# Kernel optimization log

Hardware: AMD Instinct MI355X
Metric: run time of the kernel (lower is better)

## Reference

```python
import jax, jax.numpy as jnp
import numpy as np
from jax.scipy.special import logsumexp

EPS = 0.005
MAX_ITER = 100
TOL = 1e-3
B, N, M, D = 16, 2048, 2048, 3


def setup_inputs() -> dict:
    key = jax.random.key(0)
    k1, k2 = jax.random.split(key)
    p1 = jax.random.normal(k1, (B, N, D), dtype=jnp.float32)
    p2 = jax.random.normal(k2, (B, M, D), dtype=jnp.float32)
    return {"p1": p1, "p2": p2}


def _cdist_l2(p1, p2):
    sq1 = jnp.sum(p1 * p1, axis=-1)                      # (B, N)
    sq2 = jnp.sum(p2 * p2, axis=-1)                      # (B, M)
    cross = jnp.einsum('bnd,bmd->bnm', p1, p2)           # (B, N, M)
    d2 = jnp.maximum(sq1[:, :, None] + sq2[None is None and sq2.ndim and slice(None) or 0][:, None, :] - 2.0 * cross, 0.0) if False else jnp.maximum(sq1[:, :, None] + sq2[:, None, :] - 2.0 * cross, 0.0)
    return jnp.sqrt(d2)


def reference(p1, p2):
    b_, n_, _ = p1.shape
    m_ = p2.shape[1]
    dist = _cdist_l2(p1, p2)                              # (B, N, M)
    log_a = jnp.full((b_, n_), jnp.log(1.0 / n_ + 1e-8), dtype=p1.dtype)
    log_b = jnp.full((b_, m_), jnp.log(1.0 / m_ + 1e-8), dtype=p1.dtype)
    u0 = jnp.zeros((b_, n_), dtype=p1.dtype)
    v0 = jnp.zeros((b_, m_), dtype=p1.dtype)

    def step(carry, _):
        u, v, done = carry
        u_new = EPS * (log_a - logsumexp((v[:, None, :] - dist) / EPS, axis=2))
        v_new = EPS * (log_b - logsumexp((u_new[:, :, None] - dist) / EPS, axis=1))
        conv = (jnp.max(jnp.abs(u_new - u)) < TOL) & (jnp.max(jnp.abs(v_new - v)) < TOL)
        # freeze potentials once converged (emulates the torch early break)
        u = jnp.where(done, u, u_new)
        v = jnp.where(done, v, v_new)
        return (u, v, done | conv), None

    (u, v, _), _ = jax.lax.scan(step, (u0, v0, jnp.array(False)), None, length=MAX_ITER)

    P = jnp.exp((u[:, :, None] + v[:, None, :] - dist) / EPS)  # transport plan
    emd = jnp.sum(P * dist, axis=(1, 2))                       # (B,)
    return jnp.mean(emd)
```

## Files before the change

### kernel.cpp

```cpp
#include <hip/hip_runtime.h>
#include <math.h>

namespace {
constexpr int   Bb    = 16;
constexpr int   Nn    = 2048;
constexpr int   Mm    = 2048;
constexpr float EPSf  = 0.005f;
constexpr int   MAXIT = 100;
constexpr float LN2f  = 0.69314718055994531f;
constexpr float L2Ef  = 1.44269504088896340f;
constexpr float C2f   = 288.53900817779268f;
constexpr int   BLOCK = 256;
constexpr int   RW    = 4;
constexpr int   RPB   = 16;
constexpr int   SUBS  = Nn / RPB;
constexpr int   GRID  = Bb * SUBS;
constexpr int   NCH   = 32;
}

__device__ __forceinline__ float ex2(float x) { return __builtin_amdgcn_exp2f(x); }

__global__ __launch_bounds__(BLOCK) void pack_pts(const float* __restrict__ p,
                                                  float4* __restrict__ pk, int npts) {
  int i = blockIdx.x * BLOCK + threadIdx.x;
  if (i < npts) pk[i] = make_float4(p[3 * i], p[3 * i + 1], p[3 * i + 2], 0.0f);
}

__global__ __launch_bounds__(BLOCK) void bbox_k(const float4* __restrict__ pk1,
                                                const float4* __restrict__ pk2,
                                                float4* __restrict__ bbox) {
  __shared__ float4 smin[BLOCK], smax[BLOCK];
  const int cb = blockIdx.x;
  const float4* p = (cb < 16 ? pk1 : pk2) + (cb & 15) * Nn;
  float4 mn = make_float4(3e38f, 3e38f, 3e38f, 0), mx = make_float4(-3e38f, -3e38f, -3e38f, 0);
  for (int i = threadIdx.x; i < Nn; i += BLOCK) {
    float4 v = p[i];
    mn.x = fminf(mn.x, v.x); mn.y = fminf(mn.y, v.y); mn.z = fminf(mn.z, v.z);
    mx.x = fmaxf(mx.x, v.x); mx.y = fmaxf(mx.y, v.y); mx.z = fmaxf(mx.z, v.z);
  }
  smin[threadIdx.x] = mn; smax[threadIdx.x] = mx;
  __syncthreads();
  for (int k = BLOCK / 2; k > 0; k >>= 1) {
    if (threadIdx.x < k) {
      float4 a = smin[threadIdx.x], c = smin[threadIdx.x + k];
      smin[threadIdx.x] = make_float4(fminf(a.x, c.x), fminf(a.y, c.y), fminf(a.z, c.z), 0);
      float4 d = smax[threadIdx.x], e = smax[threadIdx.x + k];
      smax[threadIdx.x] = make_float4(fmaxf(d.x, e.x), fmaxf(d.y, e.y), fmaxf(d.z, e.z), 0);
    }
    __syncthreads();
  }
  if (threadIdx.x == 0) { bbox[cb * 2] = smin[0]; bbox[cb * 2 + 1] = smax[0]; }
}

__device__ __forceinline__ unsigned spread3(unsigned v) {
  v = (v * 0x00010001u) & 0xFF0000FFu;
  v = (v * 0x00000101u) & 0x0F00F00Fu;
  v = (v * 0x00000011u) & 0xC30C30C3u;
  v = (v * 0x00000005u) & 0x49249249u;
  return v;
}

__global__ __launch_bounds__(BLOCK) void sort_k(float4* __restrict__ pk1,
                                                float4* __restrict__ pk2,
                                                const float4* __restrict__ bbox,
                                                float4* __restrict__ chunkbox) {
  __shared__ float4 pts[Nn];
  __shared__ unsigned key[Nn];
  const int cb = blockIdx.x, tid = threadIdx.x;
  float4* p = (cb < 16 ? pk1 : pk2) + (cb & 15) * Nn;
  float4 lo = bbox[cb * 2], hi = bbox[cb * 2 + 1];
  float sx = 127.0f / fmaxf(hi.x - lo.x, 1e-9f);
  float sy = 127.0f / fmaxf(hi.y - lo.y, 1e-9f);
  float sz = 127.0f / fmaxf(hi.z - lo.z, 1e-9f);
  for (int i = tid; i < Nn; i += BLOCK) {
    float4 v = p[i];
    pts[i] = v;
    unsigned qx = (unsigned)fminf(fmaxf((v.x - lo.x) * sx, 0.f), 127.f);
    unsigned qy = (unsigned)fminf(fmaxf((v.y - lo.y) * sy, 0.f), 127.f);
    unsigned qz = (unsigned)fminf(fmaxf((v.z - lo.z) * sz, 0.f), 127.f);
    unsigned m = spread3(qx) | (spread3(qy) << 1) | (spread3(qz) << 2);
    key[i] = (m << 11) | (unsigned)i;
  }
  __syncthreads();
  for (int k = 2; k <= Nn; k <<= 1)
    for (int j = k >> 1; j > 0; j >>= 1) {
      for (int t = tid; t < Nn / 2; t += BLOCK) {
        int i = ((t & ~(j - 1)) << 1) | (t & (j - 1));
        int ixj = i | j;
        bool up = ((i & k) == 0);
        unsigned a = key[i], bq = key[ixj];
        if ((a > bq) == up) { key[i] = bq; key[ixj] = a; }
      }
      __syncthreads();
    }
  float4 g[Nn / BLOCK];
  #pragma unroll
  for (int c = 0; c < Nn / BLOCK; ++c)
    g[c] = pts[key[tid + c * BLOCK] & 2047u];
  __syncthreads();
  #pragma unroll
  for (int c = 0; c < Nn / BLOCK; ++c) {
    pts[tid + c * BLOCK] = g[c];
    p[tid + c * BLOCK]   = g[c];
  }
  __syncthreads();
  const int lane = tid & 63, wid = tid >> 6;
  for (int c = wid; c < NCH; c += 4) {
    float4 v = pts[c * 64 + lane];
    float mnx = v.x, mny = v.y, mnz = v.z, mxx = v.x, mxy = v.y, mxz = v.z;
    #pragma unroll
    for (int off = 1; off < 64; off <<= 1) {
      mnx = fminf(mnx, __shfl_xor(mnx, off)); mny = fminf(mny, __shfl_xor(mny, off));
      mnz = fminf(mnz, __shfl_xor(mnz, off)); mxx = fmaxf(mxx, __shfl_xor(mxx, off));
      mxy = fmaxf(mxy, __shfl_xor(mxy, off)); mxz = fmaxf(mxz, __shfl_xor(mxz, off));
    }
    if (lane == 0) {
      chunkbox[(cb * NCH + c) * 2]     = make_float4(mnx, mny, mnz, 0);
      chunkbox[(cb * NCH + c) * 2 + 1] = make_float4(mxx, mxy, mxz, 0);
    }
  }
}

__global__ __launch_bounds__(BLOCK, 8) void sink_fast(
    const float4* __restrict__ pkc, float4* __restrict__ pkr,
    float* __restrict__ potr,
    const float4* __restrict__ cbox_cols, const float* __restrict__ cm_cols,
    float* __restrict__ cmout, float thrAdd) {
  __shared__ float redw[4];
  const int tid = threadIdx.x, lane = tid & 63, wid = tid >> 6;
  const int b = blockIdx.x >> 7, sub = blockIdx.x & 127;
  const float4* PC = pkc + b * Mm;
  float4*       PRq = pkr + b * Nn;
  float*        QR  = potr + b * Nn;

  const float log_ab = logf(1.0f / 2048.0f + 1e-8f);
  const float log2ab = log_ab * L2Ef;
  const float invC2 = 1.0f / C2f;

  const int base_n = sub * RPB + wid * RW;
  float qx[RW], qy[RW], qz[RW], K[RW], s[RW];
  #pragma unroll
  for (int r = 0; r < RW; ++r) {
    float4 q = PRq[base_n + r];
    qx[r] = q.x; qy[r] = q.y; qz[r] = q.z;
    K[r]  = log2ab - q.w;
    s[r]  = 0.0f;
  }

  unsigned msk = ~0u;
  if (thrAdd < 1e8f) {
    float4 clo = make_float4(0, 0, 0, 0), chi = clo;
    float cmw = -3.0e38f;
    if (lane < 32) {
      clo = cbox_cols[(b * NCH + lane) * 2];
      chi = cbox_cols[(b * NCH + lane) * 2 + 1];
      float4 c4 = ((const float4*)cm_cols)[b * NCH + lane];
      cmw = fmaxf(fmaxf(c4.x, c4.y), fmaxf(c4.z, c4.w));
    }
    unsigned m = 0;
    #pragma unroll
    for (int r = 0; r < RW; ++r) {
      float thr = (cmw - K[r] + thrAdd) * invC2;
      float ax = fmaxf(fmaxf(clo.x - qx[r], qx[r] - chi.x), 0.0f);
      float ay = fmaxf(fmaxf(clo.y - qy[r], qy[r] - chi.y), 0.0f);
      float az = fmaxf(fmaxf(clo.z - qz[r], qz[r] - chi.z), 0.0f);
      float d2low = fmaf(az, az, fmaf(ay, ay, ax * ax));
      bool keep = (lane < 32) && (thr > 0.0f) && (d2low <= thr * thr);
      m |= (unsigned)(__ballot(keep) & 0xFFFFFFFFull);
    }
    msk = m;
  }

  const float4* p = PC + lane;
  if (msk) {
    int j = __builtin_ctz(msk); msk &= msk - 1;
    float4 f = p[j * 64];
    for (;;) {
      float4 fn; bool more = (msk != 0);
      if (more) { int jn = __builtin_ctz(msk); msk &= msk - 1; fn = p[jn * 64]; }
      #pragma unroll
      for (int r = 0; r < RW; ++r) {
        float dx = f.x - qx[r], dy = f.y - qy[r], dz = f.z - qz[r];
        float d2 = fmaf(dz, dz, fmaf(dy, dy, dx * dx));
        s[r] += ex2(fmaf(__builtin_amdgcn_sqrtf(d2), -C2f, f.w - K[r]));
      }
      if (!more) break;
      f = fn;
    }
  }

  float* PRw = (float*)(PRq);
  float wmax = -3.0e38f;
  #pragma unroll
  for (int r = 0; r < RW; ++r) {
    float sv = s[r];
    #pragma unroll
    for (int off = 1; off < 64; off <<= 1) sv += __shfl_xor(sv, off);
    sv = fmaxf(sv, 1e-37f);
    float lse = (K[r] + __builtin_amdgcn_logf(sv)) * LN2f;
    float pnew = EPSf * (log_ab - lse);
    if (lane == 0) {
      int n = base_n + r;
      __builtin_nontemporal_store(pnew, &QR[n]);
      __builtin_nontemporal_store(pnew * C2f, &PRw[4 * n + 3]);
      wmax = fmaxf(wmax, pnew * C2f);
    }
  }
  if (lane == 0) redw[wid] = wmax;
  __syncthreads();
  if (tid == 0) {
    float m = fmaxf(fmaxf(redw[0], redw[1]), fmaxf(redw[2], redw[3]));
    __builtin_nontemporal_store(m, &cmout[(b * NCH + (sub >> 2)) * 4 + (sub & 3)]);
  }
}

__global__ __launch_bounds__(BLOCK, 8) void final_emd(
    const float4* __restrict__ pk1, const float4* __restrict__ pk2,
    const float* __restrict__ U, float* __restrict__ part) {
  __shared__ float red[4];
  const int tid = threadIdx.x, lane = tid & 63, wid = tid >> 6;
  const int b = blockIdx.x >> 7, sub = blockIdx.x & 127;
  const float4* PC = pk2 + b * Mm;
  const float4* PRq = pk1 + b * Nn;

  const int base_n = sub * RPB + wid * RW;
  float qx[RW], qy[RW], qz[RW], uc[RW], ac[RW];
  #pragma unroll
  for (int r = 0; r < RW; ++r) {
    float4 q = PRq[base_n + r];
    qx[r] = q.x; qy[r] = q.y; qz[r] = q.z;
    uc[r] = U[b * Nn + base_n + r] * C2f;
    ac[r] = 0.0f;
  }

  const float4* p = PC + lane;
  #pragma unroll 2
  for (int j = 0; j < 32; j += 4) {
    float4 f0 = p[(j + 0) * 64];
    float4 f1 = p[(j + 1) * 64];
    float4 f2 = p[(j + 2) * 64];
    float4 f3 = p[(j + 3) * 64];
    #pragma unroll
    for (int r = 0; r < RW; ++r) {
      float dx0 = f0.x - qx[r], dy0 = f0.y - qy[r], dz0 = f0.z - qz[r];
      float dx1 = f1.x - qx[r], dy1 = f1.y - qy[r], dz1 = f1.z - qz[r];
      float dx2 = f2.x - qx[r], dy2 = f2.y - qy[r], dz2 = f2.z - qz[r];
      float dx3 = f3.x - qx[r], dy3 = f3.y - qy[r], dz3 = f3.z - qz[r];
      float e0 = fmaf(dz0, dz0, fmaf(dy0, dy0, dx0 * dx0));
      float e1 = fmaf(dz1, dz1, fmaf(dy1, dy1, dx1 * dx1));
      float e2 = fmaf(dz2, dz2, fmaf(dy2, dy2, dx2 * dx2));
      float e3 = fmaf(dz3, dz3, fmaf(dy3, dy3, dx3 * dx3));
      float t0 = __builtin_amdgcn_sqrtf(e0);
      float t1 = __builtin_amdgcn_sqrtf(e1);
      float t2 = __builtin_amdgcn_sqrtf(e2);
      float t3 = __builtin_amdgcn_sqrtf(e3);
      ac[r] = fmaf(ex2(fmaf(t0, -C2f, f0.w) + uc[r]), t0, ac[r]);
      ac[r] = fmaf(ex2(fmaf(t1, -C2f, f1.w) + uc[r]), t1, ac[r]);
      ac[r] = fmaf(ex2(fmaf(t2, -C2f, f2.w) + uc[r]), t2, ac[r]);
      ac[r] = fmaf(ex2(fmaf(t3, -C2f, f3.w) + uc[r]), t3, ac[r]);
    }
  }
  float acc = 0.0f;
  #pragma unroll
  for (int r = 0; r < RW; ++r) acc += ac[r];
  #pragma unroll
  for (int off = 1; off < 64; off <<= 1) acc += __shfl_xor(acc, off);
  if (lane == 0) red[wid] = acc;
  __syncthreads();
  if (tid == 0) part[blockIdx.x] = (red[0] + red[1]) + (red[2] + red[3]);
}

__global__ __launch_bounds__(BLOCK) void write_out(const float* __restrict__ part,
                                                   float* __restrict__ out) {
  __shared__ double sd[BLOCK];
  int t = threadIdx.x;
  double s = 0.0;
  for (int i = t; i < GRID; i += BLOCK) s += (double)part[i];
  sd[t] = s;
  __syncthreads();
  for (int k = BLOCK / 2; k > 0; k >>= 1) {
    if (t < k) sd[t] += sd[t + k];
    __syncthreads();
  }
  if (t == 0) out[0] = (float)(sd[0] / (double)Bb);
}

extern "C" void kernel_launch(void* const* d_in, const int* in_sizes, int n_in,
                              void* d_out, int out_size, void* d_ws, size_t ws_size,
                              hipStream_t stream) {
  (void)in_sizes; (void)n_in; (void)out_size; (void)ws_size;
  const float* p1 = (const float*)d_in[0];
  const float* p2 = (const float*)d_in[1];
  char* ws = (char*)d_ws;
  float4*   pk1   = (float4*)(ws + 0);
  float4*   pk2   = (float4*)(ws + 524288);
  float*    U     = (float*)(ws + 1048576);
  float*    V     = (float*)(ws + 1179648);
  float*    part  = (float*)(ws + 1310720);
  float4*   bbox  = (float4*)(ws + 1318912);
  float4*   cbox  = (float4*)(ws + 1319936);
  float*    cm    = (float*)(ws + 1352704);
  float4*   cbox1 = cbox;
  float4*   cbox2 = cbox + 16 * NCH * 2;
  float*    cm1   = cm;
  float*    cm2   = cm + 16 * NCH * 4;

  const int npts = Bb * Nn;
  pack_pts<<<(npts + BLOCK - 1) / BLOCK, BLOCK, 0, stream>>>(p1, pk1, npts);
  pack_pts<<<(npts + BLOCK - 1) / BLOCK, BLOCK, 0, stream>>>(p2, pk2, npts);
  bbox_k<<<32, BLOCK, 0, stream>>>(pk1, pk2, bbox);
  sort_k<<<32, BLOCK, 0, stream>>>(pk1, pk2, bbox, cbox);

  sink_fast<<<GRID, BLOCK, 0, stream>>>(pk2, pk1, U, cbox2, cm2, cm1, 1e9f);
  sink_fast<<<GRID, BLOCK, 0, stream>>>(pk1, pk2, V, cbox1, cm1, cm2, 1e9f);
  for (int it = 1; it < MAXIT; ++it) {
    float thr = (it < 4) ? 120.0f : 48.0f;
    sink_fast<<<GRID, BLOCK, 0, stream>>>(pk2, pk1, U, cbox2, cm2, cm1, thr);
    sink_fast<<<GRID, BLOCK, 0, stream>>>(pk1, pk2, V, cbox1, cm1, cm2, thr);
  }

  final_emd<<<GRID, BLOCK, 0, stream>>>(pk1, pk2, U, part);
  write_out<<<1, BLOCK, 0, stream>>>(part, (float*)d_out);
}
```

Before: 4.582 ms.

## Double rows per wave, fuse bbox into sort, fold final reduction into EMD kernel

Raises the number of rows each wave processes from 4 to 8, which halves the grid and doubles column reuse per load. The per-block column-max bookkeeping shrinks from 4 to 2 entries per chunk to match. The separate bbox kernel is merged into the sort kernel using wave shuffles. The write_out kernel is replaced by a last-block ticket reduction inside final_emd, which removes two launches. The trade-off is higher register pressure and fewer blocks (1024) for the Sinkhorn passes, which may reduce occupancy and latency hiding.

```diff
diff --git a/kernel.cpp b/kernel.cpp
--- a/kernel.cpp
+++ b/kernel.cpp
@@ -11,8 +11,8 @@
 constexpr float L2Ef  = 1.44269504088896340f;
 constexpr float C2f   = 288.53900817779268f;
 constexpr int   BLOCK = 256;
-constexpr int   RW    = 4;
-constexpr int   RPB   = 16;
+constexpr int   RW    = 8;
+constexpr int   RPB   = 32;
 constexpr int   SUBS  = Nn / RPB;
 constexpr int   GRID  = Bb * SUBS;
 constexpr int   NCH   = 32;
@@ -24,32 +24,6 @@
                                                   float4* __restrict__ pk, int npts) {
   int i = blockIdx.x * BLOCK + threadIdx.x;
   if (i < npts) pk[i] = make_float4(p[3 * i], p[3 * i + 1], p[3 * i + 2], 0.0f);
-}
-
-__global__ __launch_bounds__(BLOCK) void bbox_k(const float4* __restrict__ pk1,
-                                                const float4* __restrict__ pk2,
-                                                float4* __restrict__ bbox) {
-  __shared__ float4 smin[BLOCK], smax[BLOCK];
-  const int cb = blockIdx.x;
-  const float4* p = (cb < 16 ? pk1 : pk2) + (cb & 15) * Nn;
-  float4 mn = make_float4(3e38f, 3e38f, 3e38f, 0), mx = make_float4(-3e38f, -3e38f, -3e38f, 0);
-  for (int i = threadIdx.x; i < Nn; i += BLOCK) {
-    float4 v = p[i];
-    mn.x = fminf(mn.x, v.x); mn.y = fminf(mn.y, v.y); mn.z = fminf(mn.z, v.z);
-    mx.x = fmaxf(mx.x, v.x); mx.y = fmaxf(mx.y, v.y); mx.z = fmaxf(mx.z, v.z);
-  }
-  smin[threadIdx.x] = mn; smax[threadIdx.x] = mx;
-  __syncthreads();
-  for (int k = BLOCK / 2; k > 0; k >>= 1) {
-    if (threadIdx.x < k) {
-      float4 a = smin[threadIdx.x], c = smin[threadIdx.x + k];
-      smin[threadIdx.x] = make_float4(fminf(a.x, c.x), fminf(a.y, c.y), fminf(a.z, c.z), 0);
-      float4 d = smax[threadIdx.x], e = smax[threadIdx.x + k];
-      smax[threadIdx.x] = make_float4(fmaxf(d.x, e.x), fmaxf(d.y, e.y), fmaxf(d.z, e.z), 0);
-    }
-    __syncthreads();
-  }
-  if (threadIdx.x == 0) { bbox[cb * 2] = smin[0]; bbox[cb * 2 + 1] = smax[0]; }
 }
 
 __device__ __forceinline__ unsigned spread3(unsigned v) {
@@ -62,22 +36,47 @@
 
 __global__ __launch_bounds__(BLOCK) void sort_k(float4* __restrict__ pk1,
                                                 float4* __restrict__ pk2,
-                                                const float4* __restrict__ bbox,
                                                 float4* __restrict__ chunkbox) {
   __shared__ float4 pts[Nn];
   __shared__ unsigned key[Nn];
+  __shared__ float rmin[3 * 4], rmax[3 * 4];
   const int cb = blockIdx.x, tid = threadIdx.x;
+  const int lane = tid & 63, wid = tid >> 6;
   float4* p = (cb < 16 ? pk1 : pk2) + (cb & 15) * Nn;
-  float4 lo = bbox[cb * 2], hi = bbox[cb * 2 + 1];
-  float sx = 127.0f / fmaxf(hi.x - lo.x, 1e-9f);
-  float sy = 127.0f / fmaxf(hi.y - lo.y, 1e-9f);
-  float sz = 127.0f / fmaxf(hi.z - lo.z, 1e-9f);
+
+  float mnx = 3e38f, mny = 3e38f, mnz = 3e38f, mxx = -3e38f, mxy = -3e38f, mxz = -3e38f;
   for (int i = tid; i < Nn; i += BLOCK) {
     float4 v = p[i];
     pts[i] = v;
-    unsigned qx = (unsigned)fminf(fmaxf((v.x - lo.x) * sx, 0.f), 127.f);
-    unsigned qy = (unsigned)fminf(fmaxf((v.y - lo.y) * sy, 0.f), 127.f);
-    unsigned qz = (unsigned)fminf(fmaxf((v.z - lo.z) * sz, 0.f), 127.f);
+    mnx = fminf(mnx, v.x); mny = fminf(mny, v.y); mnz = fminf(mnz, v.z);
+    mxx = fmaxf(mxx, v.x); mxy = fmaxf(mxy, v.y); mxz = fmaxf(mxz, v.z);
+  }
+  #pragma unroll
+  for (int off = 1; off < 64; off <<= 1) {
+    mnx = fminf(mnx, __shfl_xor(mnx, off)); mny = fminf(mny, __shfl_xor(mny, off));
+    mnz = fminf(mnz, __shfl_xor(mnz, off)); mxx = fmaxf(mxx, __shfl_xor(mxx, off));
+    mxy = fmaxf(mxy, __shfl_xor(mxy, off)); mxz = fmaxf(mxz, __shfl_xor(mxz, off));
+  }
+  if (lane == 0) {
+    rmin[wid] = mnx; rmin[4 + wid] = mny; rmin[8 + wid] = mnz;
+    rmax[wid] = mxx; rmax[4 + wid] = mxy; rmax[8 + wid] = mxz;
+  }
+  __syncthreads();
+  float lox = fminf(fminf(rmin[0], rmin[1]), fminf(rmin[2], rmin[3]));
+  float loy = fminf(fminf(rmin[4], rmin[5]), fminf(rmin[6], rmin[7]));
+  float loz = fminf(fminf(rmin[8], rmin[9]), fminf(rmin[10], rmin[11]));
+  float hix = fmaxf(fmaxf(rmax[0], rmax[1]), fmaxf(rmax[2], rmax[3]));
+  float hiy = fmaxf(fmaxf(rmax[4], rmax[5]), fmaxf(rmax[6], rmax[7]));
+  float hiz = fmaxf(fmaxf(rmax[8], rmax[9]), fmaxf(rmax[10], rmax[11]));
+  float sx = 127.0f / fmaxf(hix - lox, 1e-9f);
+  float sy = 127.0f / fmaxf(hiy - loy, 1e-9f);
+  float sz = 127.0f / fmaxf(hiz - loz, 1e-9f);
+
+  for (int i = tid; i < Nn; i += BLOCK) {
+    float4 v = pts[i];
+    unsigned qx = (unsigned)fminf(fmaxf((v.x - lox) * sx, 0.f), 127.f);
+    unsigned qy = (unsigned)fminf(fmaxf((v.y - loy) * sy, 0.f), 127.f);
+    unsigned qz = (unsigned)fminf(fmaxf((v.z - loz) * sz, 0.f), 127.f);
     unsigned m = spread3(qx) | (spread3(qy) << 1) | (spread3(qz) << 2);
     key[i] = (m << 11) | (unsigned)i;
   }
@@ -104,19 +103,18 @@
     p[tid + c * BLOCK]   = g[c];
   }
   __syncthreads();
-  const int lane = tid & 63, wid = tid >> 6;
   for (int c = wid; c < NCH; c += 4) {
     float4 v = pts[c * 64 + lane];
-    float mnx = v.x, mny = v.y, mnz = v.z, mxx = v.x, mxy = v.y, mxz = v.z;
+    float ax = v.x, ay = v.y, az = v.z, bx = v.x, by = v.y, bz = v.z;
     #pragma unroll
     for (int off = 1; off < 64; off <<= 1) {
-      mnx = fminf(mnx, __shfl_xor(mnx, off)); mny = fminf(mny, __shfl_xor(mny, off));
-      mnz = fminf(mnz, __shfl_xor(mnz, off)); mxx = fmaxf(mxx, __shfl_xor(mxx, off));
-      mxy = fmaxf(mxy, __shfl_xor(mxy, off)); mxz = fmaxf(mxz, __shfl_xor(mxz, off));
+      ax = fminf(ax, __shfl_xor(ax, off)); ay = fminf(ay, __shfl_xor(ay, off));
+      az = fminf(az, __shfl_xor(az, off)); bx = fmaxf(bx, __shfl_xor(bx, off));
+      by = fmaxf(by, __shfl_xor(by, off)); bz = fmaxf(bz, __shfl_xor(bz, off));
     }
     if (lane == 0) {
-      chunkbox[(cb * NCH + c) * 2]     = make_float4(mnx, mny, mnz, 0);
-      chunkbox[(cb * NCH + c) * 2 + 1] = make_float4(mxx, mxy, mxz, 0);
+      chunkbox[(cb * NCH + c) * 2]     = make_float4(ax, ay, az, 0);
+      chunkbox[(cb * NCH + c) * 2 + 1] = make_float4(bx, by, bz, 0);
     }
   }
 }
@@ -128,7 +126,7 @@
     float* __restrict__ cmout, float thrAdd) {
   __shared__ float redw[4];
   const int tid = threadIdx.x, lane = tid & 63, wid = tid >> 6;
-  const int b = blockIdx.x >> 7, sub = blockIdx.x & 127;
+  const int b = blockIdx.x >> 6, sub = blockIdx.x & 63;
   const float4* PC = pkc + b * Mm;
   float4*       PRq = pkr + b * Nn;
   float*        QR  = potr + b * Nn;
@@ -154,8 +152,8 @@
     if (lane < 32) {
       clo = cbox_cols[(b * NCH + lane) * 2];
       chi = cbox_cols[(b * NCH + lane) * 2 + 1];
-      float4 c4 = ((const float4*)cm_cols)[b * NCH + lane];
-      cmw = fmaxf(fmaxf(c4.x, c4.y), fmaxf(c4.z, c4.w));
+      float2 c2 = ((const float2*)cm_cols)[b * NCH + lane];
+      cmw = fmaxf(c2.x, c2.y);
     }
     unsigned m = 0;
     #pragma unroll
@@ -210,16 +208,19 @@
   __syncthreads();
   if (tid == 0) {
     float m = fmaxf(fmaxf(redw[0], redw[1]), fmaxf(redw[2], redw[3]));
-    __builtin_nontemporal_store(m, &cmout[(b * NCH + (sub >> 2)) * 4 + (sub & 3)]);
+    __builtin_nontemporal_store(m, &cmout[(b * NCH + (sub >> 1)) * 2 + (sub & 1)]);
   }
 }
 
 __global__ __launch_bounds__(BLOCK, 8) void final_emd(
     const float4* __restrict__ pk1, const float4* __restrict__ pk2,
-    const float* __restrict__ U, float* __restrict__ part) {
+    const float* __restrict__ U, float* __restrict__ part,
+    unsigned* __restrict__ ticket, float* __restrict__ out) {
   __shared__ float red[4];
+  __shared__ double sd[BLOCK];
+  __shared__ bool last;
   const int tid = threadIdx.x, lane = tid & 63, wid = tid >> 6;
-  const int b = blockIdx.x >> 7, sub = blockIdx.x & 127;
+  const int b = blockIdx.x >> 6, sub = blockIdx.x & 63;
   const float4* PC = pk2 + b * Mm;
   const float4* PRq = pk1 + b * Nn;
 
@@ -234,30 +235,19 @@
   }
 
   const float4* p = PC + lane;
-  #pragma unroll 2
-  for (int j = 0; j < 32; j += 4) {
+  for (int j = 0; j < 32; j += 2) {
     float4 f0 = p[(j + 0) * 64];
     float4 f1 = p[(j + 1) * 64];
-    float4 f2 = p[(j + 2) * 64];
-    float4 f3 = p[(j + 3) * 64];
     #pragma unroll
     for (int r = 0; r < RW; ++r) {
       float dx0 = f0.x - qx[r], dy0 = f0.y - qy[r], dz0 = f0.z - qz[r];
       float dx1 = f1.x - qx[r], dy1 = f1.y - qy[r], dz1 = f1.z - qz[r];
-      float dx2 = f2.x - qx[r], dy2 = f2.y - qy[r], dz2 = f2.z - qz[r];
-      float dx3 = f3.x - qx[r], dy3 = f3.y - qy[r], dz3 = f3.z - qz[r];
       float e0 = fmaf(dz0, dz0, fmaf(dy0, dy0, dx0 * dx0));
       float e1 = fmaf(dz1, dz1, fmaf(dy1, dy1, dx1 * dx1));
-      float e2 = fmaf(dz2, dz2, fmaf(dy2, dy2, dx2 * dx2));
-      float e3 = fmaf(dz3, dz3, fmaf(dy3, dy3, dx3 * dx3));
       float t0 = __builtin_amdgcn_sqrtf(e0);
       float t1 = __builtin_amdgcn_sqrtf(e1);
-      float t2 = __builtin_amdgcn_sqrtf(e2);
-      float t3 = __builtin_amdgcn_sqrtf(e3);
       ac[r] = fmaf(ex2(fmaf(t0, -C2f, f0.w) + uc[r]), t0, ac[r]);
       ac[r] = fmaf(ex2(fmaf(t1, -C2f, f1.w) + uc[r]), t1, ac[r]);
-      ac[r] = fmaf(ex2(fmaf(t2, -C2f, f2.w) + uc[r]), t2, ac[r]);
-      ac[r] = fmaf(ex2(fmaf(t3, -C2f, f3.w) + uc[r]), t3, ac[r]);
     }
   }
   float acc = 0.0f;
@@ -267,22 +257,29 @@
   for (int off = 1; off < 64; off <<= 1) acc += __shfl_xor(acc, off);
   if (lane == 0) red[wid] = acc;
   __syncthreads();
-  if (tid == 0) part[blockIdx.x] = (red[0] + red[1]) + (red[2] + red[3]);
-}
-
-__global__ __launch_bounds__(BLOCK) void write_out(const float* __restrict__ part,
-                                                   float* __restrict__ out) {
-  __shared__ double sd[BLOCK];
-  int t = threadIdx.x;
-  double s = 0.0;
-  for (int i = t; i < GRID; i += BLOCK) s += (double)part[i];
-  sd[t] = s;
-  __syncthreads();
-  for (int k = BLOCK / 2; k > 0; k >>= 1) {
-    if (t < k) sd[t] += sd[t + k];
+  if (tid == 0) {
+    part[blockIdx.x] = (red[0] + red[1]) + (red[2] + red[3]);
+    __builtin_amdgcn_fence(__ATOMIC_RELEASE, "agent");
+    unsigned t = __hip_atomic_fetch_add(ticket, 1u, __ATOMIC_ACQ_REL,
+                                        __HIP_MEMORY_SCOPE_AGENT);
+    last = (t == (unsigned)(GRID - 1));
+  }
+  __syncthreads();
+  if (last) {
+    __builtin_amdgcn_fence(__ATOMIC_ACQUIRE, "agent");
+    double sl = 0.0;
+    for (int i = tid; i < GRID; i += BLOCK) sl += (double)part[i];
+    sd[tid] = sl;
     __syncthreads();
-  }
-  if (t == 0) out[0] = (float)(sd[0] / (double)Bb);
+    for (int k = BLOCK / 2; k > 0; k >>= 1) {
+      if (tid < k) sd[tid] += sd[tid + k];
+      __syncthreads();
+    }
+    if (tid == 0) {
+      out[0] = (float)(sd[0] / (double)Bb);
+      __hip_atomic_store(ticket, 0u, __ATOMIC_RELAXED, __HIP_MEMORY_SCOPE_AGENT);
+    }
+  }
 }
 
 extern "C" void kernel_launch(void* const* d_in, const int* in_sizes, int n_in,
@@ -297,19 +294,19 @@
   float*    U     = (float*)(ws + 1048576);
   float*    V     = (float*)(ws + 1179648);
   float*    part  = (float*)(ws + 1310720);
-  float4*   bbox  = (float4*)(ws + 1318912);
-  float4*   cbox  = (float4*)(ws + 1319936);
-  float*    cm    = (float*)(ws + 1352704);
+  float4*   cbox  = (float4*)(ws + 1314816);
+  float*    cm    = (float*)(ws + 1347584);
+  unsigned* tick  = (unsigned*)(ws + 1355776);
   float4*   cbox1 = cbox;
   float4*   cbox2 = cbox + 16 * NCH * 2;
   float*    cm1   = cm;
-  float*    cm2   = cm + 16 * NCH * 4;
+  float*    cm2   = cm + 16 * NCH * 2;
 
   const int npts = Bb * Nn;
   pack_pts<<<(npts + BLOCK - 1) / BLOCK, BLOCK, 0, stream>>>(p1, pk1, npts);
   pack_pts<<<(npts + BLOCK - 1) / BLOCK, BLOCK, 0, stream>>>(p2, pk2, npts);
-  bbox_k<<<32, BLOCK, 0, stream>>>(pk1, pk2, bbox);
-  sort_k<<<32, BLOCK, 0, stream>>>(pk1, pk2, bbox, cbox);
+  hipMemsetAsync(tick, 0, 4, stream);
+  sort_k<<<32, BLOCK, 0, stream>>>(pk1, pk2, cbox);
 
   sink_fast<<<GRID, BLOCK, 0, stream>>>(pk2, pk1, U, cbox2, cm2, cm1, 1e9f);
   sink_fast<<<GRID, BLOCK, 0, stream>>>(pk1, pk2, V, cbox1, cm1, cm2, 1e9f);
@@ -319,6 +316,5 @@
     sink_fast<<<GRID, BLOCK, 0, stream>>>(pk1, pk2, V, cbox1, cm1, cm2, thr);
   }
 
-  final_emd<<<GRID, BLOCK, 0, stream>>>(pk1, pk2, U, part);
-  write_out<<<1, BLOCK, 0, stream>>>(part, (float*)d_out);
-}
+  final_emd<<<GRID, BLOCK, 0, stream>>>(pk1, pk2, U, part, tick, (float*)d_out);
+}
```

New measurement: 5.584 ms. 1.22x slower.
